# Optimization experiments

Hardware: AMD Instinct MI355X
Metric: run time of the kernel (lower is better)

Reference implementation:

```python
import jax, jax.numpy as jnp
import numpy as np

B, D, N, M, R, C = 512, 16, 64, 32, 32, 10  # batch, divisions, feat_in, feat_map, TR-rank, categories


def setup_inputs() -> dict:
    key = jax.random.key(0)
    k1, k2, k3, k4 = jax.random.split(key, 4)
    tensor = jax.random.normal(k1, (B, D, N), dtype=jnp.float32)
    W_fm = jax.random.normal(k2, (N, M), dtype=jnp.float32) / np.sqrt(N)
    b_fm = jax.random.normal(k3, (M,), dtype=jnp.float32) * 0.01
    # one [R, M, R] tensor-ring core per (category, division)
    G = jax.random.normal(k4, (C, D, R, M, R), dtype=jnp.float32) / np.sqrt(M * R)
    return {"tensor": tensor, "W_fm": W_fm, "b_fm": b_fm, "G": G}


def reference(tensor, W_fm, b_fm, G):
    # FeatureMap: learned linear n -> m applied per division  [B, D, M]
    feat = jnp.einsum('bdn,nm->bdm', tensor, W_fm) + b_fm
    # CoreKernelTensorRing per (category, division): [B,M] x [R,M,R] -> [B,R,R]
    cores = jnp.einsum('bdm,cdimj->cdbij', feat, G)  # [C, D, B, R, R]
    # __foward_products: chained batched matmul along divisions (structural loop, D fixed)
    prod = cores[:, 0]  # [C, B, R, R]
    for d in range(1, D):
        prod = jnp.matmul(prod, cores[:, d])
    # __calculate_traces: per-sample trace, one logit per category
    logits = jnp.einsum('cbii->bc', prod)  # [B, C]
    return jax.nn.log_softmax(logits, axis=1)
```

## Files before the change

### kernel.cpp

```cpp
#include <hip/hip_runtime.h>
#include <math.h>

#define BB 512
#define DD 16
#define NN 64
#define MM 32
#define RR 32
#define CC 10
#define BBLK 16
#define SS 2
#define DSEG (DD / SS)
#define ROWH 40
#define BREGH 1304

typedef _Float16 v8h __attribute__((ext_vector_type(8)));
typedef float v4f __attribute__((ext_vector_type(4)));

union H8 { unsigned int u[4]; v8h h; _Float16 e[8]; };
union H4 { unsigned int u[2]; _Float16 e[4]; };

__global__ __launch_bounds__(256) void produce_kernel(
    const float* __restrict__ tensor, const float* __restrict__ W,
    const float* __restrict__ bias,   const float* __restrict__ G,
    _Float16* __restrict__ fh,        _Float16* __restrict__ gh) {
    __shared__ __align__(16) char smem[36864];
    const int t = threadIdx.x;
    if (blockIdx.x < 1024) {
        float* ten_s = (float*)smem;
        float* W_s   = (float*)smem + 512;
        const int bd0 = blockIdx.x * 8;
        if (t < 128)
            *(float4*)(ten_s + t * 4) = *(const float4*)(tensor + bd0 * NN + t * 4);
        *(float4*)(W_s + t * 4)        = *(const float4*)(W + t * 4);
        *(float4*)(W_s + 1024 + t * 4) = *(const float4*)(W + 1024 + t * 4);
        __syncthreads();
        const int m = t & 31, bd_l = t >> 5;
        float acc = bias[m];
#pragma unroll
        for (int n = 0; n < NN; ++n) acc += ten_s[bd_l * NN + n] * W_s[n * MM + m];
        fh[(bd0 + bd_l) * MM + m] = (_Float16)acc;
    } else {
        _Float16* lg = (_Float16*)smem;
        const int pb = blockIdx.x - 1024;
        const int c  = pb >> 5;
        const int d  = (pb >> 1) & 15;
        const int hf = pb & 1;
        const float* src = G + (size_t)(c * DD + d) * 32768 + hf * 16384;
#pragma unroll
        for (int k = 0; k < 16; ++k) {
            const int f = (k * 256 + t) * 4;
            float4 v = *(const float4*)(src + f);
            const int di = f >> 10, m = (f >> 5) & 31, j = f & 31;
            H4 hv;
            hv.e[0] = (_Float16)v.x; hv.e[1] = (_Float16)v.y;
            hv.e[2] = (_Float16)v.z; hv.e[3] = (_Float16)v.w;
            *(uint2*)(lg + di * 1152 + m * 36 + j) = make_uint2(hv.u[0], hv.u[1]);
        }
        __syncthreads();
#pragma unroll
        for (int k = 0; k < 8; ++k) {
            const int idx = k * 256 + t;
            const int tl = idx >> 6, ln = idx & 63;
            const int di = tl >> 1, jh = tl & 1;
            const int q = ln >> 4, j4 = ln & 15;
            const int j = jh * 16 + j4;
            H8 o;
#pragma unroll
            for (int r = 0; r < 8; ++r)
                o.e[r] = lg[di * 1152 + (8 * q + r) * 36 + j];
            const size_t gi = ((size_t)(c * DD + d) * 64 + hf * 32 + tl) * 64 + ln;
            *(v8h*)(gh + gi * 8) = o.h;
        }
    }
}

__global__ __launch_bounds__(512, 4) void chain_kernel(
    const _Float16* __restrict__ feat_h,
    const _Float16* __restrict__ g_h,
    float* __restrict__ segP)
{
    __shared__ __align__(16) _Float16 lds[BBLK * BREGH];

    const int bid = blockIdx.x;
    const int xcd = bid & 7;
    const int idx = bid >> 3;
    int c, sub;
    if (idx < 64) { c = xcd; sub = idx; }
    else {
        const int e = idx - 64;
        if (xcd >= 2 && xcd <= 5) { c = 8; sub = (xcd - 2) * 16 + e; }
        else                      { c = 9; sub = (((xcd + 2) & 7)) * 16 + e; }
    }
    const int s  = sub & 1;
    const int b0 = (sub >> 1) * BBLK;
    const int d0 = s * DSEG;
    const int t    = threadIdx.x;
    const int w    = t >> 6;
    const int lane = t & 63;
    const int q    = lane >> 4;
    const int j4   = lane & 15;

    const int bA = b0 + j4;
    const size_t gc = (size_t)c * DD * 32768;

    v8h afh = *(const v8h*)(feat_h + (size_t)bA * (DD * MM) + d0 * MM + q * 8);
    v8h gf[8];
#pragma unroll
    for (int u = 0; u < 8; ++u)
        gf[u] = *(const v8h*)(g_h + gc + (size_t)d0 * 32768 +
                              ((size_t)(w * 8 + u) * 64 + lane) * 8);

    v8h pah[2][2];

    for (int dd = 0; dd < DSEG; ++dd) {
        const int d = d0 + dd;
        __syncthreads();
        v4f av[8];
#pragma unroll
        for (int u = 0; u < 8; ++u) {
            v4f z = {0.f, 0.f, 0.f, 0.f};
            av[u] = __builtin_amdgcn_mfma_f32_16x16x32_f16(afh, gf[u], z, 0, 0, 0);
        }
        if (dd < DSEG - 1) {
            afh = *(const v8h*)(feat_h + (size_t)bA * (DD * MM) + (d + 1) * MM + q * 8);
            const size_t gb = gc + (size_t)(d + 1) * 32768;
#pragma unroll
            for (int u = 0; u < 8; ++u)
                gf[u] = *(const v8h*)(g_h + gb + ((size_t)(w * 8 + u) * 64 + lane) * 8);
        }
#pragma unroll
        for (int jh = 0; jh < 2; ++jh)
#pragma unroll
            for (int reg = 0; reg < 4; ++reg) {
                H4 hv;
                hv.e[0] = (_Float16)av[0 + jh][reg];
                hv.e[1] = (_Float16)av[2 + jh][reg];
                hv.e[2] = (_Float16)av[4 + jh][reg];
                hv.e[3] = (_Float16)av[6 + jh][reg];
                *(uint2*)(&lds[(4 * q + reg) * BREGH + (16 * jh + j4) * ROWH + 4 * w]) =
                    make_uint2(hv.u[0], hv.u[1]);
            }
        __syncthreads();
#pragma unroll
        for (int cc = 0; cc < 2; ++cc) {
            const int bl = 2 * w + cc;
            _Float16* base = lds + bl * BREGH;
            if (dd == 0) {
#pragma unroll
                for (int mi = 0; mi < 2; ++mi) {
                    H8 a;
#pragma unroll
                    for (int r = 0; r < 8; ++r)
                        a.e[r] = base[(8 * q + r) * ROWH + 16 * mi + j4];
                    pah[cc][mi] = a.h;
                }
            } else {
                v8h bf[2];
#pragma unroll
                for (int ni = 0; ni < 2; ++ni)
                    bf[ni] = *(const v8h*)(base + (16 * ni + j4) * ROWH + 8 * q);
                v4f acc[2][2];
#pragma unroll
                for (int mi = 0; mi < 2; ++mi)
#pragma unroll
                    for (int ni = 0; ni < 2; ++ni) {
                        v4f z = {0.f, 0.f, 0.f, 0.f};
                        acc[mi][ni] = __builtin_amdgcn_mfma_f32_16x16x32_f16(
                            pah[cc][mi], bf[ni], z, 0, 0, 0);
                    }
                if (dd < DSEG - 1) {
#pragma unroll
                    for (int mi = 0; mi < 2; ++mi)
#pragma unroll
                        for (int ni = 0; ni < 2; ++ni)
#pragma unroll
                            for (int reg = 0; reg < 4; ++reg)
                                base[(16 * mi + 4 * q + reg) * ROWH + 16 * ni + j4] =
                                    (_Float16)acc[mi][ni][reg];
                    __builtin_amdgcn_sched_barrier(0);
#pragma unroll
                    for (int mi = 0; mi < 2; ++mi)
                        pah[cc][mi] = *(const v8h*)(base + (16 * mi + j4) * ROWH + 8 * q);
                } else {
                    float* dst = segP + ((size_t)s * CC * BB +
                                         (size_t)c * BB + (b0 + bl)) * 1024;
                    if (s == 0) {
#pragma unroll
                        for (int mi = 0; mi < 2; ++mi)
#pragma unroll
                            for (int ni = 0; ni < 2; ++ni)
#pragma unroll
                                for (int reg = 0; reg < 4; ++reg)
                                    dst[(16 * mi + 4 * q + reg) * 32 + 16 * ni + j4] =
                                        acc[mi][ni][reg];
                    } else {
#pragma unroll
                        for (int mi = 0; mi < 2; ++mi)
#pragma unroll
                            for (int ni = 0; ni < 2; ++ni)
#pragma unroll
                                for (int reg = 0; reg < 4; ++reg)
                                    dst[(16 * ni + j4) * 32 + 16 * mi + 4 * q + reg] =
                                        acc[mi][ni][reg];
                    }
                }
            }
        }
    }
}

__global__ __launch_bounds__(256) void combine_lsm_kernel(
    const float* __restrict__ segP, float* __restrict__ out) {
    const int t    = threadIdx.x;
    const int b    = blockIdx.x * 4 + (t >> 6);
    const int lane = t & 63;
    const float* P1b = segP + (size_t)CC * BB * 1024;

    float tr[CC];
#pragma unroll
    for (int c = 0; c < CC; ++c) {
        const float* p0 = segP + ((size_t)c * BB + b) * 1024 + lane * 16;
        const float* p1 = P1b  + ((size_t)c * BB + b) * 1024 + lane * 16;
        float acc = 0.f;
#pragma unroll
        for (int v = 0; v < 4; ++v) {
            float4 x = ((const float4*)p0)[v];
            float4 y = ((const float4*)p1)[v];
            acc += x.x * y.x + x.y * y.y + x.z * y.z + x.w * y.w;
        }
#pragma unroll
        for (int off = 32; off > 0; off >>= 1)
            acc += __shfl_xor(acc, off);
        tr[c] = acc;
    }
    float mx = -1e30f;
#pragma unroll
    for (int c = 0; c < CC; ++c) mx = fmaxf(mx, tr[c]);
    float ssum = 0.f;
#pragma unroll
    for (int c = 0; c < CC; ++c) ssum += expf(tr[c] - mx);
    const float ls = logf(ssum);
    float val = 0.f;
#pragma unroll
    for (int c = 0; c < CC; ++c) if (lane == c) val = tr[c] - mx - ls;
    if (lane < CC) out[b * CC + lane] = val;
}

extern "C" void kernel_launch(void* const* d_in, const int* in_sizes, int n_in,
                              void* d_out, int out_size, void* d_ws, size_t ws_size,
                              hipStream_t stream) {
    const float* tensor = (const float*)d_in[0];
    const float* W      = (const float*)d_in[1];
    const float* bias   = (const float*)d_in[2];
    const float* G      = (const float*)d_in[3];
    float* out = (float*)d_out;

    const size_t FEAT = (size_t)BB * DD * MM;
    const size_t GPK  = (size_t)CC * DD * 64 * 64 * 8;
    _Float16* fh = (_Float16*)d_ws;
    _Float16* gh = fh + FEAT;
    float* segP  = (float*)(gh + GPK);

    produce_kernel<<<1024 + 320, 256, 0, stream>>>(tensor, W, bias, G, fh, gh);
    chain_kernel<<<CC * (BB / BBLK) * SS, 512, 0, stream>>>(fh, gh, segP);
    combine_lsm_kernel<<<BB / 4, 256, 0, stream>>>(segP, out);
}
```

Baseline: 120.7 us.

## Run full division chain per block and fuse trace into chain kernel

Each block now processes all 16 divisions instead of half. It stashes the first-half product in registers and computes the trace in-kernel as a dot product against the second-half product. This removes the large fp32 segment-product buffer and its combine pass, leaving only a small log-softmax kernel. The cost is half as many blocks and a twice-longer serial chain per block, plus extra fp16 rounding of the stashed product.

```diff
diff --git a/kernel.cpp b/kernel.cpp
--- a/kernel.cpp
+++ b/kernel.cpp
@@ -8,8 +8,6 @@
 #define RR 32
 #define CC 10
 #define BBLK 16
-#define SS 2
-#define DSEG (DD / SS)
 #define ROWH 40
 #define BREGH 1304
 
@@ -77,7 +75,7 @@
 __global__ __launch_bounds__(512, 4) void chain_kernel(
     const _Float16* __restrict__ feat_h,
     const _Float16* __restrict__ g_h,
-    float* __restrict__ segP)
+    float* __restrict__ trout)
 {
     __shared__ __align__(16) _Float16 lds[BBLK * BREGH];
 
@@ -85,15 +83,13 @@
     const int xcd = bid & 7;
     const int idx = bid >> 3;
     int c, sub;
-    if (idx < 64) { c = xcd; sub = idx; }
+    if (idx < 32) { c = xcd; sub = idx; }
     else {
-        const int e = idx - 64;
-        if (xcd >= 2 && xcd <= 5) { c = 8; sub = (xcd - 2) * 16 + e; }
-        else                      { c = 9; sub = (((xcd + 2) & 7)) * 16 + e; }
-    }
-    const int s  = sub & 1;
-    const int b0 = (sub >> 1) * BBLK;
-    const int d0 = s * DSEG;
+        const int e = idx - 32;
+        if (xcd >= 2 && xcd <= 5) { c = 8; sub = (xcd - 2) * 8 + e; }
+        else                      { c = 9; sub = (((xcd + 2) & 7)) * 8 + e; }
+    }
+    const int b0 = sub * BBLK;
     const int t    = threadIdx.x;
     const int w    = t >> 6;
     const int lane = t & 63;
@@ -103,17 +99,16 @@
     const int bA = b0 + j4;
     const size_t gc = (size_t)c * DD * 32768;
 
-    v8h afh = *(const v8h*)(feat_h + (size_t)bA * (DD * MM) + d0 * MM + q * 8);
+    v8h afh = *(const v8h*)(feat_h + (size_t)bA * (DD * MM) + 0 * MM + q * 8);
     v8h gf[8];
 #pragma unroll
     for (int u = 0; u < 8; ++u)
-        gf[u] = *(const v8h*)(g_h + gc + (size_t)d0 * 32768 +
-                              ((size_t)(w * 8 + u) * 64 + lane) * 8);
-
-    v8h pah[2][2];
-
-    for (int dd = 0; dd < DSEG; ++dd) {
-        const int d = d0 + dd;
+        gf[u] = *(const v8h*)(g_h + gc + ((size_t)(w * 8 + u) * 64 + lane) * 8);
+
+    v8h sb[2][2];
+    uint2 p0u[2][2][2];
+
+    for (int d = 0; d < DD; ++d) {
         __syncthreads();
         v4f av[8];
 #pragma unroll
@@ -121,7 +116,7 @@
             v4f z = {0.f, 0.f, 0.f, 0.f};
             av[u] = __builtin_amdgcn_mfma_f32_16x16x32_f16(afh, gf[u], z, 0, 0, 0);
         }
-        if (dd < DSEG - 1) {
+        if (d < DD - 1) {
             afh = *(const v8h*)(feat_h + (size_t)bA * (DD * MM) + (d + 1) * MM + q * 8);
             const size_t gb = gc + (size_t)(d + 1) * 32768;
 #pragma unroll
@@ -145,63 +140,76 @@
         for (int cc = 0; cc < 2; ++cc) {
             const int bl = 2 * w + cc;
             _Float16* base = lds + bl * BREGH;
-            if (dd == 0) {
-#pragma unroll
-                for (int mi = 0; mi < 2; ++mi) {
-                    H8 a;
+            if (d == 0 || d == 8) {
+#pragma unroll
+                for (int vt = 0; vt < 2; ++vt) {
+                    H8 x;
 #pragma unroll
                     for (int r = 0; r < 8; ++r)
-                        a.e[r] = base[(8 * q + r) * ROWH + 16 * mi + j4];
-                    pah[cc][mi] = a.h;
+                        x.e[r] = base[(8 * q + r) * ROWH + 16 * vt + j4];
+                    sb[cc][vt] = x.h;
                 }
             } else {
-                v8h bf[2];
-#pragma unroll
-                for (int ni = 0; ni < 2; ++ni)
-                    bf[ni] = *(const v8h*)(base + (16 * ni + j4) * ROWH + 8 * q);
+                v8h af2[2];
+#pragma unroll
+                for (int jt = 0; jt < 2; ++jt)
+                    af2[jt] = *(const v8h*)(base + (16 * jt + j4) * ROWH + 8 * q);
                 v4f acc[2][2];
 #pragma unroll
-                for (int mi = 0; mi < 2; ++mi)
-#pragma unroll
-                    for (int ni = 0; ni < 2; ++ni) {
+                for (int jt = 0; jt < 2; ++jt)
+#pragma unroll
+                    for (int vt = 0; vt < 2; ++vt) {
                         v4f z = {0.f, 0.f, 0.f, 0.f};
-                        acc[mi][ni] = __builtin_amdgcn_mfma_f32_16x16x32_f16(
-                            pah[cc][mi], bf[ni], z, 0, 0, 0);
+                        acc[jt][vt] = __builtin_amdgcn_mfma_f32_16x16x32_f16(
+                            af2[jt], sb[cc][vt], z, 0, 0, 0);
                     }
-                if (dd < DSEG - 1) {
-#pragma unroll
-                    for (int mi = 0; mi < 2; ++mi)
-#pragma unroll
-                        for (int ni = 0; ni < 2; ++ni)
+                if (d == DD - 1) {
+                    float ts = 0.f;
+#pragma unroll
+                    for (int jt = 0; jt < 2; ++jt)
+#pragma unroll
+                        for (int vt = 0; vt < 2; ++vt) {
+                            H4 pv;
+                            pv.u[0] = p0u[cc][jt][vt].x;
+                            pv.u[1] = p0u[cc][jt][vt].y;
 #pragma unroll
                             for (int reg = 0; reg < 4; ++reg)
-                                base[(16 * mi + 4 * q + reg) * ROWH + 16 * ni + j4] =
-                                    (_Float16)acc[mi][ni][reg];
+                                ts += acc[jt][vt][reg] * (float)pv.e[reg];
+                        }
+#pragma unroll
+                    for (int off = 32; off > 0; off >>= 1)
+                        ts += __shfl_xor(ts, off);
+                    if (lane == 0) trout[(size_t)(b0 + bl) * CC + c] = ts;
+                } else {
+#pragma unroll
+                    for (int jt = 0; jt < 2; ++jt)
+#pragma unroll
+                        for (int vt = 0; vt < 2; ++vt) {
+                            H4 hv;
+                            hv.e[0] = (_Float16)acc[jt][vt][0];
+                            hv.e[1] = (_Float16)acc[jt][vt][1];
+                            hv.e[2] = (_Float16)acc[jt][vt][2];
+                            hv.e[3] = (_Float16)acc[jt][vt][3];
+                            *(uint2*)(base + (16 * vt + j4) * ROWH + 16 * jt + 4 * q) =
+                                make_uint2(hv.u[0], hv.u[1]);
+                        }
                     __builtin_amdgcn_sched_barrier(0);
-#pragma unroll
-                    for (int mi = 0; mi < 2; ++mi)
-                        pah[cc][mi] = *(const v8h*)(base + (16 * mi + j4) * ROWH + 8 * q);
-                } else {
-                    float* dst = segP + ((size_t)s * CC * BB +
-                                         (size_t)c * BB + (b0 + bl)) * 1024;
-                    if (s == 0) {
-#pragma unroll
-                        for (int mi = 0; mi < 2; ++mi)
-#pragma unroll
-                            for (int ni = 0; ni < 2; ++ni)
+                    if (d == 7) {
+#pragma unroll
+                        for (int jt = 0; jt < 2; ++jt)
+#pragma unroll
+                            for (int vt = 0; vt < 2; ++vt) {
+                                H4 pv;
 #pragma unroll
                                 for (int reg = 0; reg < 4; ++reg)
-                                    dst[(16 * mi + 4 * q + reg) * 32 + 16 * ni + j4] =
-                                        acc[mi][ni][reg];
+                                    pv.e[reg] =
+                                        base[(16 * jt + 4 * q + reg) * ROWH + 16 * vt + j4];
+                                p0u[cc][jt][vt] = make_uint2(pv.u[0], pv.u[1]);
+                            }
                     } else {
 #pragma unroll
-                        for (int mi = 0; mi < 2; ++mi)
-#pragma unroll
-                            for (int ni = 0; ni < 2; ++ni)
-#pragma unroll
-                                for (int reg = 0; reg < 4; ++reg)
-                                    dst[(16 * ni + j4) * 32 + 16 * mi + 4 * q + reg] =
-                                        acc[mi][ni][reg];
+                        for (int vt = 0; vt < 2; ++vt)
+                            sb[cc][vt] = *(const v8h*)(base + (16 * vt + j4) * ROWH + 8 * q);
                     }
                 }
             }
@@ -209,41 +217,22 @@
     }
 }
 
-__global__ __launch_bounds__(256) void combine_lsm_kernel(
-    const float* __restrict__ segP, float* __restrict__ out) {
-    const int t    = threadIdx.x;
-    const int b    = blockIdx.x * 4 + (t >> 6);
-    const int lane = t & 63;
-    const float* P1b = segP + (size_t)CC * BB * 1024;
-
-    float tr[CC];
+__global__ __launch_bounds__(256) void lsm_kernel(
+    const float* __restrict__ tr, float* __restrict__ out) {
+    const int b = blockIdx.x * 256 + threadIdx.x;
+    float v[CC];
+    float mx = -1e30f;
 #pragma unroll
     for (int c = 0; c < CC; ++c) {
-        const float* p0 = segP + ((size_t)c * BB + b) * 1024 + lane * 16;
-        const float* p1 = P1b  + ((size_t)c * BB + b) * 1024 + lane * 16;
-        float acc = 0.f;
-#pragma unroll
-        for (int v = 0; v < 4; ++v) {
-            float4 x = ((const float4*)p0)[v];
-            float4 y = ((const float4*)p1)[v];
-            acc += x.x * y.x + x.y * y.y + x.z * y.z + x.w * y.w;
-        }
-#pragma unroll
-        for (int off = 32; off > 0; off >>= 1)
-            acc += __shfl_xor(acc, off);
-        tr[c] = acc;
-    }
-    float mx = -1e30f;
-#pragma unroll
-    for (int c = 0; c < CC; ++c) mx = fmaxf(mx, tr[c]);
+        v[c] = tr[b * CC + c];
+        mx = fmaxf(mx, v[c]);
+    }
     float ssum = 0.f;
 #pragma unroll
-    for (int c = 0; c < CC; ++c) ssum += expf(tr[c] - mx);
+    for (int c = 0; c < CC; ++c) ssum += expf(v[c] - mx);
     const float ls = logf(ssum);
-    float val = 0.f;
-#pragma unroll
-    for (int c = 0; c < CC; ++c) if (lane == c) val = tr[c] - mx - ls;
-    if (lane < CC) out[b * CC + lane] = val;
+#pragma unroll
+    for (int c = 0; c < CC; ++c) out[b * CC + c] = v[c] - mx - ls;
 }
 
 extern "C" void kernel_launch(void* const* d_in, const int* in_sizes, int n_in,
@@ -259,9 +248,9 @@
     const size_t GPK  = (size_t)CC * DD * 64 * 64 * 8;
     _Float16* fh = (_Float16*)d_ws;
     _Float16* gh = fh + FEAT;
-    float* segP  = (float*)(gh + GPK);
+    float* trbuf = (float*)(gh + GPK);
 
     produce_kernel<<<1024 + 320, 256, 0, stream>>>(tensor, W, bias, G, fh, gh);
-    chain_kernel<<<CC * (BB / BBLK) * SS, 512, 0, stream>>>(fh, gh, segP);
-    combine_lsm_kernel<<<BB / 4, 256, 0, stream>>>(segP, out);
-}
+    chain_kernel<<<CC * (BB / BBLK), 512, 0, stream>>>(fh, gh, trbuf);
+    lsm_kernel<<<BB / 256, 256, 0, stream>>>(trbuf, out);
+}
```

Result: slower. 152.8 us (+26.6%).
